# Performance work log

Hardware: AMD Instinct MI355X
Metric: run time of the kernel (lower is better)

Reference implementation:

```python
import jax, jax.numpy as jnp
import numpy as np

B, T, C, H = 2, 2048, 2048, 16
D = C // H  # head_dim = 128
SCALE = 1.0 / np.sqrt(D)


def setup_inputs() -> dict:
    key = jax.random.key(0)
    ks = jax.random.split(key, 9)
    x = jax.random.normal(ks[0], (B, T, C), dtype=jnp.float32)
    # additive causal mask [T, T]
    attn_mask = jnp.where(jnp.tril(jnp.ones((T, T), dtype=bool)), 0.0, -1e9).astype(jnp.float32)
    s_cc = 1.0 / np.sqrt(C)
    s_cd = 1.0 / np.sqrt(C)
    Wq = jax.random.normal(ks[1], (C, C), dtype=jnp.float32) * s_cc
    Wk = jax.random.normal(ks[2], (D, C), dtype=jnp.float32) * s_cd
    Wv = jax.random.normal(ks[3], (D, C), dtype=jnp.float32) * s_cd
    Wo = jax.random.normal(ks[4], (C, C), dtype=jnp.float32) * s_cc
    bq = jnp.zeros((C,), jnp.float32)
    bk = jnp.zeros((D,), jnp.float32)
    bv = jnp.zeros((D,), jnp.float32)
    bo = jnp.zeros((C,), jnp.float32)
    return {"x": x, "attn_mask": attn_mask, "Wq": Wq, "bq": bq, "Wk": Wk,
            "bk": bk, "Wv": Wv, "bv": bv, "Wo": Wo, "bo": bo}


def reference(x, attn_mask, Wq, bq, Wk, bk, Wv, bv, Wo, bo):
    # projections (torch Linear: x @ W.T + b)
    q = (x @ Wq.T + bq).reshape(B, T, H, D).transpose(0, 2, 1, 3)  # [B,H,T,D]
    k = x @ Wk.T + bk                                              # [B,T,D] single KV head
    v = x @ Wv.T + bv                                              # [B,T,D]
    # scores: broadcast shared K over all H query heads
    scores = jnp.einsum('bhtd,bsd->bhts', q, k) * SCALE            # [B,H,T,T]
    scores = scores + attn_mask  # [T,T] broadcasts over B,H
    attn = jax.nn.softmax(scores, axis=-1)
    out = jnp.einsum('bhts,bsd->bhtd', attn, v)                    # [B,H,T,D]
    out = out.transpose(0, 2, 1, 3).reshape(B, T, C)
    return out @ Wo.T + bo
```

## Files before the change

### kernel.cpp

```cpp
#include <hip/hip_runtime.h>
#include <stdint.h>

typedef unsigned short u16;
typedef __attribute__((ext_vector_type(8))) __bf16 bf16x8;
typedef __attribute__((ext_vector_type(4))) __bf16 bf16x4;
typedef __attribute__((ext_vector_type(4))) float f32x4;
typedef __attribute__((ext_vector_type(8))) u16 u16x8;
typedef __attribute__((ext_vector_type(4))) short s16x4;
typedef __attribute__((ext_vector_type(2))) unsigned int u32x2;

#define B_SZ 2
#define T_SZ 2048
#define C_SZ 2048
#define H_SZ 16
#define D_SZ 128
#define NQKV 2304
#define ATT_SCALE 0.08838834764831845f
#define LOG2E_SCALE 0.12751744f
#define DEFER_THR 90.50967f

typedef __attribute__((address_space(1))) void* as1_void_p;
typedef __attribute__((address_space(3))) void* as3_void_p;

__device__ __forceinline__ u16 f2b(float f) {
  union { float f; uint32_t u; } c; c.f = f;
  return (u16)((c.u + 0x7FFFu + ((c.u >> 16) & 1u)) >> 16);
}

__device__ __forceinline__ void gload_lds16(const u16* g, u16* l) {
  __builtin_amdgcn_global_load_lds((as1_void_p)g, (as3_void_p)l, 16, 0, 0);
}

__device__ __forceinline__ f32x4 mfma16(s16x4 a, s16x4 b, f32x4 c) {
#if __has_builtin(__builtin_amdgcn_mfma_f32_16x16x16bf16_1k)
  return __builtin_amdgcn_mfma_f32_16x16x16bf16_1k(a, b, c, 0, 0, 0);
#elif __has_builtin(__builtin_amdgcn_mfma_f32_16x16x16_bf16)
  return __builtin_amdgcn_mfma_f32_16x16x16_bf16(
      __builtin_bit_cast(bf16x4, a), __builtin_bit_cast(bf16x4, b), c, 0, 0, 0);
#else
  u32x2 ua = __builtin_bit_cast(u32x2, a);
  u32x2 ub = __builtin_bit_cast(u32x2, b);
  asm("s_nop 1\n\tv_mfma_f32_16x16x16_bf16 %0, %1, %2, %0\n\ts_nop 7"
      : "+v"(c) : "v"(ua), "v"(ub));
  return c;
#endif
}

__device__ __forceinline__ void cast4(const float* __restrict__ in,
                                      u16* __restrict__ out, int lb, int tid) {
  int idx = lb * 1024 + tid * 4;
  float4 f = *(const float4*)&in[idx];
  ushort4 o4;
  o4.x = f2b(f.x); o4.y = f2b(f.y); o4.z = f2b(f.z); o4.w = f2b(f.w);
  *(ushort4*)&out[idx] = o4;
}

__global__ __launch_bounds__(256) void prep(const float* __restrict__ x,
                                            const float* __restrict__ Wq,
                                            const float* __restrict__ Wk,
                                            const float* __restrict__ Wv,
                                            const float* __restrict__ Wo,
                                            const float* __restrict__ bq,
                                            const float* __restrict__ bk,
                                            const float* __restrict__ bv,
                                            u16* __restrict__ xb,
                                            u16* __restrict__ wqkv,
                                            u16* __restrict__ wob,
                                            float* __restrict__ bqkv) {
  const int bid = blockIdx.x, tid = threadIdx.x;
  if (bid < 8192)       cast4(x,  xb,              bid,         tid);
  else if (bid < 12288) cast4(Wq, wqkv,            bid - 8192,  tid);
  else if (bid < 12544) cast4(Wk, wqkv + 4194304,  bid - 12288, tid);
  else if (bid < 12800) cast4(Wv, wqkv + 4456448,  bid - 12544, tid);
  else if (bid < 16896) cast4(Wo, wob,             bid - 12800, tid);
  else {
    int e = (bid - 16896) * 1024 + tid * 4;
#pragma unroll
    for (int j = 0; j < 4; j++) {
      int i = e + j;
      if (i < NQKV)
        bqkv[i] = i < C_SZ ? bq[i] : (i < C_SZ + D_SZ ? bk[i - C_SZ] : bv[i - C_SZ - D_SZ]);
    }
  }
}

template <typename OutT>
__global__ __launch_bounds__(256) void gemm_bt(const u16* __restrict__ A,
                                               const u16* __restrict__ Bm,
                                               const float* __restrict__ bias,
                                               OutT* __restrict__ C,
                                               int K, int ldc) {
  __shared__ u16 lsA[2][128 * 32];
  __shared__ u16 lsB[2][128 * 32];
  const int tid = threadIdx.x;
  const int lane = tid & 63;
  const int wave = tid >> 6;
  const int wr = wave >> 1, wc = wave & 1;
  const int l16 = lane & 15, lq = lane >> 4;
  const int nwg = gridDim.x * gridDim.y;
  int wg = blockIdx.y * gridDim.x + blockIdx.x;
  wg = (wg & 7) * (nwg >> 3) + (wg >> 3);
  const int brow = (wg / gridDim.x) * 128;
  const int bcol = (wg % gridDim.x) * 128;

  f32x4 acc[4][4] = {};

  auto STAGE = [&](int k0, int bs) {
#pragma unroll
    for (int i = 0; i < 2; i++) {
      const int woff = (i * 4 + wave) * 512;
      const int eoff = woff + lane * 8;
      const int r = eoff >> 5, c = eoff & 31;
      gload_lds16(A + (size_t)(brow + r) * K + k0 + c, &lsA[bs][woff]);
      gload_lds16(Bm + (size_t)(bcol + r) * K + k0 + c, &lsB[bs][woff]);
    }
  };

  STAGE(0, 0);
  __syncthreads();
  int cur = 0;
  for (int k0 = 0; k0 < K; k0 += 32) {
    if (k0 + 32 < K) STAGE(k0 + 32, cur ^ 1);

    bf16x8 af[4], bfr[4];
#pragma unroll
    for (int mi = 0; mi < 4; mi++)
      af[mi] = *(const bf16x8*)&lsA[cur][(wr * 64 + mi * 16 + l16) * 32 + lq * 8];
#pragma unroll
    for (int ni = 0; ni < 4; ni++)
      bfr[ni] = *(const bf16x8*)&lsB[cur][(wc * 64 + ni * 16 + l16) * 32 + lq * 8];
#pragma unroll
    for (int mi = 0; mi < 4; mi++)
#pragma unroll
      for (int ni = 0; ni < 4; ni++)
        acc[mi][ni] = __builtin_amdgcn_mfma_f32_16x16x32_bf16(af[mi], bfr[ni], acc[mi][ni], 0, 0, 0);

    __syncthreads();
    cur ^= 1;
  }

#pragma unroll
  for (int mi = 0; mi < 4; mi++)
#pragma unroll
    for (int ni = 0; ni < 4; ni++) {
      const int col = bcol + wc * 64 + ni * 16 + l16;
      const float bb = bias ? bias[col] : 0.0f;
#pragma unroll
      for (int r = 0; r < 4; r++) {
        const int row = brow + wr * 64 + mi * 16 + lq * 4 + r;
        const float v = acc[mi][ni][r] + bb;
        if constexpr (sizeof(OutT) == 2) {
          ((u16*)C)[(size_t)row * ldc + col] = f2b(v);
        } else {
          ((float*)C)[(size_t)row * ldc + col] = v;
        }
      }
    }
}

__global__ __launch_bounds__(256) void transpose_v(const u16* __restrict__ qkv,
                                                   u16* __restrict__ vT) {
  __shared__ u16 tile[64 * 136];
  const int tid = threadIdx.x;
  const int t0 = blockIdx.x * 64;
  const int b = blockIdx.y;
#pragma unroll
  for (int i = 0; i < 4; i++) {
    int idx = (i * 256 + tid) * 8;
    int r = idx >> 7, c = idx & 127;
    u16x8 v = *(const u16x8*)&qkv[(size_t)(b * T_SZ + t0 + r) * NQKV + (C_SZ + D_SZ) + c];
    *(u16x8*)&tile[r * 136 + c] = v;
  }
  __syncthreads();
#pragma unroll
  for (int i = 0; i < 4; i++) {
    int idx = (i * 256 + tid) * 8;
    int d = idx >> 6, t = idx & 63;
    u16x8 v;
#pragma unroll
    for (int j = 0; j < 8; j++) v[j] = tile[(t + j) * 136 + d];
    *(u16x8*)&vT[(size_t)(b * D_SZ + d) * T_SZ + t0 + t] = v;
  }
}

__device__ __forceinline__ void qk_part(const u16* lk, const bf16x8 (&aq)[4],
                                        f32x4 (&s)[4], int l16, int lq) {
#pragma unroll
  for (int kk = 0; kk < 4; kk++) {
#pragma unroll
    for (int nb = 0; nb < 4; nb++) {
      const int row = nb * 16 + l16;
      const bf16x8 kf = *(const bf16x8*)&lk[row * 128 + (((kk * 4 + lq) ^ (row & 7)) << 3)];
      s[nb] = __builtin_amdgcn_mfma_f32_16x16x32_bf16(kf, aq[kk], s[nb], 0, 0, 0);
    }
  }
}

template <bool DIAG>
__device__ __forceinline__ void sm_pv(const u16* lv, f32x4 (&s)[4], f32x4 (&o)[8],
                                      float& lp, float& m, int q_rel, int l16, int lq) {
  if (DIAG) {
#pragma unroll
    for (int nb = 0; nb < 4; nb++)
#pragma unroll
      for (int rr = 0; rr < 4; rr++)
        if (nb * 16 + lq * 4 + rr > q_rel) s[nb][rr] -= 1e9f;
  }
  float m0 = fmaxf(fmaxf(s[0][0], s[0][1]), fmaxf(s[0][2], s[0][3]));
  float m1 = fmaxf(fmaxf(s[1][0], s[1][1]), fmaxf(s[1][2], s[1][3]));
  float m2 = fmaxf(fmaxf(s[2][0], s[2][1]), fmaxf(s[2][2], s[2][3]));
  float m3 = fmaxf(fmaxf(s[3][0], s[3][1]), fmaxf(s[3][2], s[3][3]));
  float mx = fmaxf(fmaxf(m0, m1), fmaxf(m2, m3));
  mx = fmaxf(mx, __shfl_xor(mx, 16, 64));
  mx = fmaxf(mx, __shfl_xor(mx, 32, 64));
  if (__any(mx > m + DEFER_THR)) {
    const float mnew = fmaxf(m, mx);
    const float alpha = exp2f((m - mnew) * LOG2E_SCALE);
    m = mnew;
    lp *= alpha;
#pragma unroll
    for (int nd = 0; nd < 8; nd++)
#pragma unroll
      for (int e = 0; e < 4; e++) o[nd][e] *= alpha;
  }
#pragma unroll
  for (int nb = 0; nb < 4; nb++) {
    bf16x4 pbv;
#pragma unroll
    for (int e = 0; e < 4; e++) {
      const float p = exp2f((s[nb][e] - m) * LOG2E_SCALE);
      lp += p;
      pbv[e] = (__bf16)p;
    }
    const s16x4 pb = __builtin_bit_cast(s16x4, pbv);
#pragma unroll
    for (int nd = 0; nd < 8; nd++) {
      const int row = nd * 16 + l16;
      const s16x4 av = *(const s16x4*)&lv[row * 64 +
          ((((nb << 1) | (lq >> 1)) ^ (row & 7)) << 3) + ((lq & 1) << 2)];
      o[nd] = mfma16(av, pb, o[nd]);
    }
  }
}

__global__ __launch_bounds__(512, 4) void attn_fwd(const u16* __restrict__ qkv,
                                                   const u16* __restrict__ vT,
                                                   u16* __restrict__ out) {
  __shared__ u16 lsK[2][64 * 128];
  __shared__ u16 lsV[2][128 * 64];
  const int tid = threadIdx.x;
  const int wv = tid >> 6, lane = tid & 63;
  const int l16 = lane & 15, lq = lane >> 4;
  const int h = blockIdx.y;
  const int b = blockIdx.z;
  const int qH = (b == 0) ? (31 - blockIdx.x) : (16 + blockIdx.x);
  const int qL = 31 - qH;
  const int bT = b * T_SZ;
  const int qt = (wv < 4) ? qH : qL;
  const int wq0 = qt * 64 + (wv & 3) * 16;

  bf16x8 aq[4];
  {
    const size_t qrow = (size_t)(bT + wq0 + l16) * NQKV + h * D_SZ;
#pragma unroll
    for (int kk = 0; kk < 4; kk++)
      aq[kk] = *(const bf16x8*)&qkv[qrow + kk * 32 + lq * 8];
  }

  f32x4 o[8] = {};
  float lp = 0.f, m = -INFINITY;

  const u16 *kp0, *kp1, *vp0, *vp1;
  {
    const int kr0 = tid >> 4,         kc0 = tid & 15;
    const int kr1 = (512 + tid) >> 4, kc1 = tid & 15;
    kp0 = qkv + (size_t)(bT + kr0) * NQKV + C_SZ + (size_t)((kc0 ^ (kr0 & 7)) * 8);
    kp1 = qkv + (size_t)(bT + kr1) * NQKV + C_SZ + (size_t)((kc1 ^ (kr1 & 7)) * 8);
    const int vr0 = tid >> 3,         vc0 = tid & 7;
    const int vr1 = (512 + tid) >> 3, vc1 = tid & 7;
    vp0 = vT + (size_t)(b * D_SZ + vr0) * T_SZ + (vc0 ^ (vr0 & 7)) * 8;
    vp1 = vT + (size_t)(b * D_SZ + vr1) * T_SZ + (vc1 ^ (vr1 & 7)) * 8;
  }
  const int kd0 = wv * 512, kd1 = (8 + wv) * 512;

  auto STAGE_K = [&](int kt, int bf) {
    const size_t off = (size_t)kt * (64 * NQKV);
    gload_lds16(kp0 + off, &lsK[bf][kd0]);
    gload_lds16(kp1 + off, &lsK[bf][kd1]);
  };
  auto STAGE_V = [&](int kt, int bf) {
    const int off = kt * 64;
    gload_lds16(vp0 + off, &lsV[bf][kd0]);
    gload_lds16(vp1 + off, &lsV[bf][kd1]);
  };

  const int nkt = qH + 1;
  STAGE_K(0, 0);
  STAGE_V(0, 0);
  __syncthreads();
  int cur = 0;
  for (int kt = 0; kt < nkt; kt++) {
    if (kt + 1 < nkt) {
      STAGE_K(kt + 1, cur ^ 1);
      STAGE_V(kt + 1, cur ^ 1);
    }
    if (kt <= qt) {
      f32x4 s[4] = {};
      qk_part(lsK[cur], aq, s, l16, lq);
      if (kt < qt)
        sm_pv<false>(lsV[cur], s, o, lp, m, 0, l16, lq);
      else
        sm_pv<true>(lsV[cur], s, o, lp, m, wq0 + l16 - kt * 64, l16, lq);
    }
    asm volatile("s_waitcnt vmcnt(0)" ::: "memory");
    __builtin_amdgcn_sched_barrier(0);
    __builtin_amdgcn_s_barrier();
    cur ^= 1;
  }

  lp += __shfl_xor(lp, 16, 64);
  lp += __shfl_xor(lp, 32, 64);
  const float r = __builtin_amdgcn_rcpf(lp);
  const size_t rowb = (size_t)(bT + wq0 + l16) * C_SZ + h * D_SZ;
#pragma unroll
  for (int nd = 0; nd < 8; nd++) {
    ushort4 sv;
    sv.x = f2b(o[nd][0] * r); sv.y = f2b(o[nd][1] * r);
    sv.z = f2b(o[nd][2] * r); sv.w = f2b(o[nd][3] * r);
    *(ushort4*)&out[rowb + nd * 16 + lq * 4] = sv;
  }
}

extern "C" void kernel_launch(void* const* d_in, const int* in_sizes, int n_in,
                              void* d_out, int out_size, void* d_ws, size_t ws_size,
                              hipStream_t stream) {
  const float* x  = (const float*)d_in[0];
  const float* Wq = (const float*)d_in[2];
  const float* bq = (const float*)d_in[3];
  const float* Wk = (const float*)d_in[4];
  const float* bk = (const float*)d_in[5];
  const float* Wv = (const float*)d_in[6];
  const float* bv = (const float*)d_in[7];
  const float* Wo = (const float*)d_in[8];
  const float* bo = (const float*)d_in[9];
  float* out = (float*)d_out;

  char* ws = (char*)d_ws;
  if (ws_size < 71312384) return;
  u16* xb     = (u16*)(ws + 0);
  u16* wqkv   = (u16*)(ws + 16777216);
  u16* wob    = (u16*)(ws + 26214400);
  u16* qkv    = (u16*)(ws + 34603008);
  u16* vT     = (u16*)(ws + 53477376);
  u16* ao     = (u16*)(ws + 54525952);
  float* bqkv = (float*)(ws + 71303168);

  prep<<<16899, 256, 0, stream>>>(x, Wq, Wk, Wv, Wo, bq, bk, bv, xb, wqkv, wob, bqkv);

  gemm_bt<u16><<<dim3(18, 32), 256, 0, stream>>>(xb, wqkv, bqkv, qkv, 2048, NQKV);
  transpose_v<<<dim3(32, 2), 256, 0, stream>>>(qkv, vT);
  attn_fwd<<<dim3(16, 16, 2), 512, 0, stream>>>(qkv, vT, ao);
  gemm_bt<float><<<dim3(16, 32), 256, 0, stream>>>(ao, wob, bo, out, 2048, 2048);
}
```

Baseline: 205.2 us.

## Process two 16-row query tiles per wave to reuse K/V LDS fragments

Each wave now handles 32 query rows as two 16-row sub-tiles (A and B) instead of one, so every K and V fragment read from LDS feeds two MFMAs. The block shrinks from 8 to 4 waves (512 to 256 threads), and each thread issues four async global-to-LDS loads per K/V tile instead of two. This halves LDS read traffic per MFMA and gives more independent MFMA chains, at the cost of doubled accumulator registers (two O accumulators) and lower occupancy via launch bounds (256, 2).

After: 229.9 us. 1.12x slower.

```diff
diff --git a/kernel.cpp b/kernel.cpp
--- a/kernel.cpp
+++ b/kernel.cpp
@@ -183,22 +183,26 @@
   }
 }
 
-__device__ __forceinline__ void qk_part(const u16* lk, const bf16x8 (&aq)[4],
-                                        f32x4 (&s)[4], int l16, int lq) {
+__device__ __forceinline__ void qk2(const u16* lk,
+                                    const bf16x8 (&aqA)[4], const bf16x8 (&aqB)[4],
+                                    f32x4 (&sA)[4], f32x4 (&sB)[4],
+                                    int l16, int lq) {
 #pragma unroll
   for (int kk = 0; kk < 4; kk++) {
 #pragma unroll
     for (int nb = 0; nb < 4; nb++) {
       const int row = nb * 16 + l16;
       const bf16x8 kf = *(const bf16x8*)&lk[row * 128 + (((kk * 4 + lq) ^ (row & 7)) << 3)];
-      s[nb] = __builtin_amdgcn_mfma_f32_16x16x32_bf16(kf, aq[kk], s[nb], 0, 0, 0);
+      sA[nb] = __builtin_amdgcn_mfma_f32_16x16x32_bf16(kf, aqA[kk], sA[nb], 0, 0, 0);
+      sB[nb] = __builtin_amdgcn_mfma_f32_16x16x32_bf16(kf, aqB[kk], sB[nb], 0, 0, 0);
     }
   }
 }
 
 template <bool DIAG>
-__device__ __forceinline__ void sm_pv(const u16* lv, f32x4 (&s)[4], f32x4 (&o)[8],
-                                      float& lp, float& m, int q_rel, int l16, int lq) {
+__device__ __forceinline__ void sm_pack(f32x4 (&s)[4], f32x4 (&o)[8],
+                                        float& lp, float& m, s16x4 (&pb)[4],
+                                        int q_rel, int l16, int lq) {
   if (DIAG) {
 #pragma unroll
     for (int nb = 0; nb < 4; nb++)
@@ -232,18 +236,28 @@
       lp += p;
       pbv[e] = (__bf16)p;
     }
-    const s16x4 pb = __builtin_bit_cast(s16x4, pbv);
+    pb[nb] = __builtin_bit_cast(s16x4, pbv);
+  }
+}
+
+__device__ __forceinline__ void pv2(const u16* lv,
+                                    const s16x4 (&pbA)[4], const s16x4 (&pbB)[4],
+                                    f32x4 (&oA)[8], f32x4 (&oB)[8],
+                                    int l16, int lq) {
+#pragma unroll
+  for (int nb = 0; nb < 4; nb++) {
 #pragma unroll
     for (int nd = 0; nd < 8; nd++) {
       const int row = nd * 16 + l16;
       const s16x4 av = *(const s16x4*)&lv[row * 64 +
           ((((nb << 1) | (lq >> 1)) ^ (row & 7)) << 3) + ((lq & 1) << 2)];
-      o[nd] = mfma16(av, pb, o[nd]);
-    }
-  }
-}
-
-__global__ __launch_bounds__(512, 4) void attn_fwd(const u16* __restrict__ qkv,
+      oA[nd] = mfma16(av, pbA[nb], oA[nd]);
+      oB[nd] = mfma16(av, pbB[nb], oB[nd]);
+    }
+  }
+}
+
+__global__ __launch_bounds__(256, 2) void attn_fwd(const u16* __restrict__ qkv,
                                                    const u16* __restrict__ vT,
                                                    u16* __restrict__ out) {
   __shared__ u16 lsK[2][64 * 128];
@@ -256,42 +270,47 @@
   const int qH = (b == 0) ? (31 - blockIdx.x) : (16 + blockIdx.x);
   const int qL = 31 - qH;
   const int bT = b * T_SZ;
-  const int qt = (wv < 4) ? qH : qL;
-  const int wq0 = qt * 64 + (wv & 3) * 16;
-
-  bf16x8 aq[4];
+  const int qt = (wv < 2) ? qH : qL;
+  const int wq0 = qt * 64 + (wv & 1) * 32;
+
+  bf16x8 aqA[4], aqB[4];
   {
-    const size_t qrow = (size_t)(bT + wq0 + l16) * NQKV + h * D_SZ;
-#pragma unroll
-    for (int kk = 0; kk < 4; kk++)
-      aq[kk] = *(const bf16x8*)&qkv[qrow + kk * 32 + lq * 8];
-  }
-
-  f32x4 o[8] = {};
-  float lp = 0.f, m = -INFINITY;
-
-  const u16 *kp0, *kp1, *vp0, *vp1;
-  {
-    const int kr0 = tid >> 4,         kc0 = tid & 15;
-    const int kr1 = (512 + tid) >> 4, kc1 = tid & 15;
-    kp0 = qkv + (size_t)(bT + kr0) * NQKV + C_SZ + (size_t)((kc0 ^ (kr0 & 7)) * 8);
-    kp1 = qkv + (size_t)(bT + kr1) * NQKV + C_SZ + (size_t)((kc1 ^ (kr1 & 7)) * 8);
-    const int vr0 = tid >> 3,         vc0 = tid & 7;
-    const int vr1 = (512 + tid) >> 3, vc1 = tid & 7;
-    vp0 = vT + (size_t)(b * D_SZ + vr0) * T_SZ + (vc0 ^ (vr0 & 7)) * 8;
-    vp1 = vT + (size_t)(b * D_SZ + vr1) * T_SZ + (vc1 ^ (vr1 & 7)) * 8;
-  }
-  const int kd0 = wv * 512, kd1 = (8 + wv) * 512;
+    const size_t rA = (size_t)(bT + wq0 + l16) * NQKV + h * D_SZ;
+    const size_t rB = rA + (size_t)16 * NQKV;
+#pragma unroll
+    for (int kk = 0; kk < 4; kk++) {
+      aqA[kk] = *(const bf16x8*)&qkv[rA + kk * 32 + lq * 8];
+      aqB[kk] = *(const bf16x8*)&qkv[rB + kk * 32 + lq * 8];
+    }
+  }
+
+  f32x4 oA[8] = {}, oB[8] = {};
+  float lpA = 0.f, lpB = 0.f;
+  float mA = -INFINITY, mB = -INFINITY;
+
+  const u16* kp[4];
+  const u16* vp[4];
+#pragma unroll
+  for (int j = 0; j < 4; j++) {
+    const int cK = (j * 4 + wv) * 64 + lane;
+    const int krow = cK >> 4, kcol = cK & 15;
+    kp[j] = qkv + (size_t)(bT + krow) * NQKV + C_SZ + (size_t)((kcol ^ (krow & 7)) * 8);
+    const int cV = (j * 4 + wv) * 64 + lane;
+    const int vrow = cV >> 3, vcol = cV & 7;
+    vp[j] = vT + (size_t)(b * D_SZ + vrow) * T_SZ + (vcol ^ (vrow & 7)) * 8;
+  }
 
   auto STAGE_K = [&](int kt, int bf) {
     const size_t off = (size_t)kt * (64 * NQKV);
-    gload_lds16(kp0 + off, &lsK[bf][kd0]);
-    gload_lds16(kp1 + off, &lsK[bf][kd1]);
+#pragma unroll
+    for (int j = 0; j < 4; j++)
+      gload_lds16(kp[j] + off, &lsK[bf][(j * 4 + wv) * 512]);
   };
   auto STAGE_V = [&](int kt, int bf) {
     const int off = kt * 64;
-    gload_lds16(vp0 + off, &lsV[bf][kd0]);
-    gload_lds16(vp1 + off, &lsV[bf][kd1]);
+#pragma unroll
+    for (int j = 0; j < 4; j++)
+      gload_lds16(vp[j] + off, &lsV[bf][(j * 4 + wv) * 512]);
   };
 
   const int nkt = qH + 1;
@@ -305,12 +324,18 @@
       STAGE_V(kt + 1, cur ^ 1);
     }
     if (kt <= qt) {
-      f32x4 s[4] = {};
-      qk_part(lsK[cur], aq, s, l16, lq);
-      if (kt < qt)
-        sm_pv<false>(lsV[cur], s, o, lp, m, 0, l16, lq);
-      else
-        sm_pv<true>(lsV[cur], s, o, lp, m, wq0 + l16 - kt * 64, l16, lq);
+      f32x4 sA[4] = {}, sB[4] = {};
+      qk2(lsK[cur], aqA, aqB, sA, sB, l16, lq);
+      s16x4 pbA[4], pbB[4];
+      if (kt < qt) {
+        sm_pack<false>(sA, oA, lpA, mA, pbA, 0, l16, lq);
+        sm_pack<false>(sB, oB, lpB, mB, pbB, 0, l16, lq);
+      } else {
+        const int qr = wq0 + l16 - kt * 64;
+        sm_pack<true>(sA, oA, lpA, mA, pbA, qr, l16, lq);
+        sm_pack<true>(sB, oB, lpB, mB, pbB, qr + 16, l16, lq);
+      }
+      pv2(lsV[cur], pbA, pbB, oA, oB, l16, lq);
     }
     asm volatile("s_waitcnt vmcnt(0)" ::: "memory");
     __builtin_amdgcn_sched_barrier(0);
@@ -318,16 +343,21 @@
     cur ^= 1;
   }
 
-  lp += __shfl_xor(lp, 16, 64);
-  lp += __shfl_xor(lp, 32, 64);
-  const float r = __builtin_amdgcn_rcpf(lp);
-  const size_t rowb = (size_t)(bT + wq0 + l16) * C_SZ + h * D_SZ;
+  lpA += __shfl_xor(lpA, 16, 64); lpA += __shfl_xor(lpA, 32, 64);
+  lpB += __shfl_xor(lpB, 16, 64); lpB += __shfl_xor(lpB, 32, 64);
+  const float rA = __builtin_amdgcn_rcpf(lpA);
+  const float rB = __builtin_amdgcn_rcpf(lpB);
+  const size_t rowbA = (size_t)(bT + wq0 + l16) * C_SZ + h * D_SZ;
+  const size_t rowbB = rowbA + (size_t)16 * C_SZ;
 #pragma unroll
   for (int nd = 0; nd < 8; nd++) {
-    ushort4 sv;
-    sv.x = f2b(o[nd][0] * r); sv.y = f2b(o[nd][1] * r);
-    sv.z = f2b(o[nd][2] * r); sv.w = f2b(o[nd][3] * r);
-    *(ushort4*)&out[rowb + nd * 16 + lq * 4] = sv;
+    ushort4 svA, svB;
+    svA.x = f2b(oA[nd][0] * rA); svA.y = f2b(oA[nd][1] * rA);
+    svA.z = f2b(oA[nd][2] * rA); svA.w = f2b(oA[nd][3] * rA);
+    svB.x = f2b(oB[nd][0] * rB); svB.y = f2b(oB[nd][1] * rB);
+    svB.z = f2b(oB[nd][2] * rB); svB.w = f2b(oB[nd][3] * rB);
+    *(ushort4*)&out[rowbA + nd * 16 + lq * 4] = svA;
+    *(ushort4*)&out[rowbB + nd * 16 + lq * 4] = svB;
   }
 }
 
@@ -359,6 +389,6 @@
 
   gemm_bt<u16><<<dim3(18, 32), 256, 0, stream>>>(xb, wqkv, bqkv, qkv, 2048, NQKV);
   transpose_v<<<dim3(32, 2), 256, 0, stream>>>(qkv, vT);
-  attn_fwd<<<dim3(16, 16, 2), 512, 0, stream>>>(qkv, vT, ao);
+  attn_fwd<<<dim3(16, 16, 2), 256, 0, stream>>>(qkv, vT, ao);
   gemm_bt<float><<<dim3(16, 32), 256, 0, stream>>>(ao, wob, bo, out, 2048, 2048);
 }
```
